# Performance work log

Hardware: AMD Instinct MI355X
Metric: run time of the kernel (lower is better)

## Reference

```python
import jax, jax.numpy as jnp
import numpy as np

N_NODES = 50000
N_EDGES = 800000
F_IN = 128
HEADS = 4
C_OUT = 32
NEG_SLOPE = 0.2
BN_EPS = 1e-5


def _add_self_loops(edge_index, edge_attr, n):
    # PyG fill_value='mean': self-loop attr = mean of incoming edge attrs per node (0 if none)
    src, dst = edge_index[0], edge_index[1]
    deg = jax.ops.segment_sum(jnp.ones_like(edge_attr[:, 0]), dst, num_segments=n)
    loop_attr = jax.ops.segment_sum(edge_attr, dst, num_segments=n) / jnp.maximum(deg, 1.0)[:, None]
    loop = jnp.arange(n)
    src2 = jnp.concatenate([src, loop])
    dst2 = jnp.concatenate([dst, loop])
    attr2 = jnp.concatenate([edge_attr, loop_attr], axis=0)
    return src2, dst2, attr2


def _segment_softmax(logits, seg, n):
    m = jax.ops.segment_max(logits, seg, num_segments=n)
    m = jnp.where(jnp.isfinite(m), m, 0.0)
    ex = jnp.exp(logits - m[seg])
    s = jax.ops.segment_sum(ex, seg, num_segments=n)
    return ex / s[seg]


def _gatv2(x, src, dst, eattr, Wl, bl, Wr, br, We, att, bias, n):
    # x: [n, F]; returns [n, HEADS*C_OUT]
    xl = (x @ Wl + bl).reshape(n, HEADS, C_OUT)
    xr = (x @ Wr + br).reshape(n, HEADS, C_OUT)
    ea = (eattr @ We).reshape(-1, HEADS, C_OUT)
    xlj = xl[src]                                   # [E, H, C] gather
    msg = jax.nn.leaky_relu(xlj + xr[dst] + ea, NEG_SLOPE)
    logits = jnp.einsum('ehc,hc->eh', msg, att)     # [E, H]
    alpha = _segment_softmax(logits, dst, n)
    out = jax.ops.segment_sum(xlj * alpha[..., None], dst, num_segments=n)
    return out.reshape(n, HEADS * C_OUT) + bias


def _batchnorm(x, gamma, beta):
    mu = x.mean(axis=0)
    var = x.var(axis=0)
    return gamma * (x - mu) * jax.lax.rsqrt(var + BN_EPS) + beta


def setup_inputs() -> dict:
    key = jax.random.key(0)
    ks = jax.random.split(key, 20)
    HC = HEADS * C_OUT
    s = 0.05
    inp = {
        'emb': jax.random.normal(ks[0], (N_NODES, F_IN), dtype=jnp.float32),
        'edge_index': jax.random.randint(ks[1], (2, N_EDGES), 0, N_NODES, dtype=jnp.int64),
        'edge_weight': jax.random.uniform(ks[2], (N_EDGES, 1), dtype=jnp.float32),
        'Wl1': jax.random.normal(ks[3], (F_IN, HC)) * s,
        'bl1': jnp.zeros((HC,), jnp.float32),
        'Wr1': jax.random.normal(ks[4], (F_IN, HC)) * s,
        'br1': jnp.zeros((HC,), jnp.float32),
        'We1': jax.random.normal(ks[5], (1, HC)) * s,
        'att1': jax.random.normal(ks[6], (HEADS, C_OUT)) * s,
        'bias1': jnp.zeros((HC,), jnp.float32),
        'gamma1': jnp.ones((HC,), jnp.float32),
        'beta1': jnp.zeros((HC,), jnp.float32),
        'Wl2': jax.random.normal(ks[7], (HC, HC)) * s,
        'bl2': jnp.zeros((HC,), jnp.float32),
        'Wr2': jax.random.normal(ks[8], (HC, HC)) * s,
        'br2': jnp.zeros((HC,), jnp.float32),
        'We2': jax.random.normal(ks[9], (1, HC)) * s,
        'att2': jax.random.normal(ks[10], (HEADS, C_OUT)) * s,
        'bias2': jnp.zeros((HC,), jnp.float32),
    }
    return inp


def reference(emb, edge_index, edge_weight, Wl1, bl1, Wr1, br1, We1, att1, bias1,
              gamma1, beta1, Wl2, bl2, Wr2, br2, We2, att2, bias2):
    n = emb.shape[0]
    src, dst, eattr = _add_self_loops(edge_index, edge_weight, n)
    h1 = _gatv2(emb, src, dst, eattr, Wl1, bl1, Wr1, br1, We1, att1, bias1, n)
    h1 = jax.nn.elu(_batchnorm(h1, gamma1, beta1))
    h2 = _gatv2(h1, src, dst, eattr, Wl2, bl2, Wr2, br2, We2, att2, bias2, n)
    # fusion: mean over [input_emb, h1, h2] along stacked axis
    return (emb + h1 + h2) / 3.0
```

## Files before the change

kernel.cpp:

```cpp
#include <hip/hip_runtime.h>
#include <hip/hip_bf16.h>
#include <math.h>

#define N_NODES 50000
#define N_EDGES 800000
#define HC 128
#define SLOT 64

#define BM 128
#define NBX ((N_NODES + BM - 1) / BM)

typedef short bh8 __attribute__((ext_vector_type(8)));
typedef float f4 __attribute__((ext_vector_type(4)));

__device__ __forceinline__ unsigned int pk2(float a, float b) {
  return (unsigned int)__bfloat16_as_ushort(__float2bfloat16(a)) |
         ((unsigned int)__bfloat16_as_ushort(__float2bfloat16(b)) << 16);
}

__global__ void k_wprep(const float* __restrict__ Wl1, const float* __restrict__ Wr1,
                        const float* __restrict__ Wl2, const float* __restrict__ Wr2,
                        unsigned short* __restrict__ WtAll) {
  int m = blockIdx.y;
  const float* src = (m == 0) ? Wl1 : (m == 1) ? Wr1 : (m == 2) ? Wl2 : Wr2;
  int idx = blockIdx.x * 256 + threadIdx.x;
  int k = idx >> 7, n = idx & 127;
  float v = src[k * HC + n];
  WtAll[((size_t)m * HC + n) * HC + k] = __bfloat16_as_ushort(__float2bfloat16(v));
}

__global__ void k_bucket(const int* __restrict__ ei, const float* __restrict__ ew,
                         int* __restrict__ cursor, int2* __restrict__ slots) {
  int e = blockIdx.x * blockDim.x + threadIdx.x;
  if (e >= N_EDGES) return;
  int s = ei[e];
  int d = ei[N_EDGES + e];
  float w = ew[e];
  int pos = atomicAdd(cursor + d, 1);
  if (pos < SLOT) {
    slots[(size_t)d * SLOT + pos] = make_int2(s, __float_as_int(w));
  }
}

template <int LAYER2>
__global__ __launch_bounds__(256) void k_gemm_mfma(
    const float* __restrict__ X, const unsigned short* __restrict__ Wt,
    const float* __restrict__ b0, const float* __restrict__ b1,
    unsigned short* __restrict__ Y0b, float* __restrict__ Y1,
    const float* __restrict__ scp, const float* __restrict__ shp) {
  __shared__ __align__(16) unsigned short Xls[128 * 128];
  __shared__ __align__(16) unsigned short Wls[128 * 128];
  int tid = threadIdx.x;
  int row0 = blockIdx.x * BM;
  {
    int r = tid >> 1;
    int ks = (tid & 1) * 64;
    int gr = row0 + r;
    const float* xp = X + (size_t)gr * HC + ks;
    int sw = r & 15;
#pragma unroll
    for (int i = 0; i < 4; ++i) {
      float f[16];
      if (gr < N_NODES) {
        *(float4*)&f[0] = *(const float4*)(xp + i * 16);
        *(float4*)&f[4] = *(const float4*)(xp + i * 16 + 4);
        *(float4*)&f[8] = *(const float4*)(xp + i * 16 + 8);
        *(float4*)&f[12] = *(const float4*)(xp + i * 16 + 12);
      } else {
#pragma unroll
        for (int j = 0; j < 16; ++j) f[j] = 0.f;
      }
      if (LAYER2) {
        float sc[16], sh[16];
#pragma unroll
        for (int q = 0; q < 4; ++q) {
          *(float4*)&sc[q * 4] = *(const float4*)(scp + ks + i * 16 + q * 4);
          *(float4*)&sh[q * 4] = *(const float4*)(shp + ks + i * 16 + q * 4);
        }
#pragma unroll
        for (int j = 0; j < 16; ++j) {
          float y = fmaf(f[j], sc[j], sh[j]);
          f[j] = (y > 0.f) ? y : (__expf(y) - 1.f);
        }
      }
      int kg = (ks >> 3) + i * 2;
      *(uint4*)&Xls[r * 128 + ((kg ^ sw) * 8)] =
          make_uint4(pk2(f[0], f[1]), pk2(f[2], f[3]), pk2(f[4], f[5]), pk2(f[6], f[7]));
      *(uint4*)&Xls[r * 128 + (((kg + 1) ^ sw) * 8)] =
          make_uint4(pk2(f[8], f[9]), pk2(f[10], f[11]), pk2(f[12], f[13]), pk2(f[14], f[15]));
    }
  }
  int lane = tid & 63;
  int wv = tid >> 6;
  int lrow = lane & 15;
  int lq = lane >> 4;
  int rbase = wv * 32;
#pragma unroll
  for (int half = 0; half < 2; ++half) {
    if (half) __syncthreads();
    {
      int n = tid >> 1;
      int ks = (tid & 1) * 64;
      const unsigned short* wp = Wt + half * (HC * HC) + n * HC + ks;
      int swn = n & 15;
#pragma unroll
      for (int g = 0; g < 8; ++g) {
        uint4 v = *(const uint4*)(wp + g * 8);
        int kg = (ks >> 3) + g;
        *(uint4*)&Wls[n * 128 + ((kg ^ swn) * 8)] = v;
      }
    }
    __syncthreads();
    f4 acc[2][8];
#pragma unroll
    for (int mt = 0; mt < 2; ++mt)
#pragma unroll
      for (int nt = 0; nt < 8; ++nt) acc[mt][nt] = (f4){0.f, 0.f, 0.f, 0.f};
#pragma unroll
    for (int kk = 0; kk < 4; ++kk) {
      int kg = kk * 4 + lq;
      bh8 a0 = *(const bh8*)&Xls[(rbase + lrow) * 128 + ((kg ^ lrow) * 8)];
      bh8 a1 = *(const bh8*)&Xls[(rbase + 16 + lrow) * 128 + ((kg ^ lrow) * 8)];
#pragma unroll
      for (int nt = 0; nt < 8; ++nt) {
        bh8 b = *(const bh8*)&Wls[(nt * 16 + lrow) * 128 + ((kg ^ lrow) * 8)];
        acc[0][nt] = __builtin_amdgcn_mfma_f32_16x16x32_bf16(a0, b, acc[0][nt], 0, 0, 0);
        acc[1][nt] = __builtin_amdgcn_mfma_f32_16x16x32_bf16(a1, b, acc[1][nt], 0, 0, 0);
      }
    }
    const float* bb = half ? b1 : b0;
    float bv[8];
#pragma unroll
    for (int nt = 0; nt < 8; ++nt) bv[nt] = bb[nt * 16 + lrow];
#pragma unroll
    for (int mt = 0; mt < 2; ++mt) {
#pragma unroll
      for (int rr = 0; rr < 4; ++rr) {
        int gr = row0 + rbase + mt * 16 + lq * 4 + rr;
        if (gr < N_NODES) {
          if (half == 0) {
#pragma unroll
            for (int nt = 0; nt < 8; ++nt)
              Y0b[(size_t)gr * HC + nt * 16 + lrow] =
                  __bfloat16_as_ushort(__float2bfloat16(acc[mt][nt][rr] + bv[nt]));
          } else {
#pragma unroll
            for (int nt = 0; nt < 8; ++nt)
              Y1[(size_t)gr * HC + nt * 16 + lrow] = acc[mt][nt][rr] + bv[nt];
          }
        }
      }
    }
  }
}

template <int FINAL>
__global__ __launch_bounds__(256) void k_gat(
    const unsigned short* __restrict__ xlb, const float* __restrict__ xr,
    const int* __restrict__ cursor, const int2* __restrict__ slots,
    const float* __restrict__ We, const float* __restrict__ att,
    const float* __restrict__ bias,
    float* __restrict__ out,
    const float* __restrict__ emb, const float* __restrict__ h1p,
    const float* __restrict__ scp, const float* __restrict__ shp) {
  int g = threadIdx.x >> 5;
  int lane = threadIdx.x & 31;
  int n = blockIdx.x * 8 + g;
  if (n >= N_NODES) return;
  int fi = n * 32 + lane;
  const uint2* xl4 = (const uint2*)xlb;
  float4 xr4 = ((const float4*)xr)[fi];
  float4 we4 = ((const float4*)We)[lane];
  float4 at4 = ((const float4*)att)[lane];
  int deg = min(cursor[n], SLOT);
  int jb = n * SLOT;
  int je = jb + deg;
  float l = 0.f, wsum = 0.f;
  float4 o = make_float4(0.f, 0.f, 0.f, 0.f);

  auto core = [&](float w, uint2 gc) {
    float4 xlj;
    xlj.x = __uint_as_float(gc.x << 16);
    xlj.y = __uint_as_float(gc.x & 0xffff0000u);
    xlj.z = __uint_as_float(gc.y << 16);
    xlj.w = __uint_as_float(gc.y & 0xffff0000u);
    float4 v;
    v.x = fmaf(w, we4.x, xlj.x + xr4.x);
    v.y = fmaf(w, we4.y, xlj.y + xr4.y);
    v.z = fmaf(w, we4.z, xlj.z + xr4.z);
    v.w = fmaf(w, we4.w, xlj.w + xr4.w);
    v.x = fmaxf(v.x, 0.2f * v.x);
    v.y = fmaxf(v.y, 0.2f * v.y);
    v.z = fmaxf(v.z, 0.2f * v.z);
    v.w = fmaxf(v.w, 0.2f * v.w);
    float p = v.x * at4.x + v.y * at4.y + v.z * at4.z + v.w * at4.w;
    p += __shfl_xor(p, 1);
    p += __shfl_xor(p, 2);
    p += __shfl_xor(p, 4);
    float e = __expf(p);
    l += e;
    o.x = fmaf(e, xlj.x, o.x);
    o.y = fmaf(e, xlj.y, o.y);
    o.z = fmaf(e, xlj.z, o.z);
    o.w = fmaf(e, xlj.w, o.w);
  };
  auto body = [&](int2 ec, uint2 gc) {
    float w = __int_as_float(ec.y);
    wsum += w;
    core(w, gc);
  };
  auto ld = [&](int j, int2& e, uint2& gq) {
    int idx = min(j, je - 1);
    e = slots[idx];
    gq = xl4[(size_t)e.x * 32 + lane];
  };

  if (deg > 0) {
    int2 e0, e1, e2, e3;
    uint2 g0, g1, g2, g3;
    ld(jb + 0, e0, g0);
    ld(jb + 1, e1, g1);
    ld(jb + 2, e2, g2);
    ld(jb + 3, e3, g3);
    for (int j = jb; j < je; j += 4) {
      int2 t0 = e0, t1 = e1, t2 = e2, t3 = e3;
      uint2 u0 = g0, u1 = g1, u2 = g2, u3 = g3;
      ld(j + 4, e0, g0);
      ld(j + 5, e1, g1);
      ld(j + 6, e2, g2);
      ld(j + 7, e3, g3);
      body(t0, u0);
      if (j + 1 < je) body(t1, u1);
      if (j + 2 < je) body(t2, u2);
      if (j + 3 < je) body(t3, u3);
    }
  }
  {
    float wself = (deg > 0) ? wsum / (float)deg : 0.f;
    uint2 gs = xl4[(size_t)n * 32 + lane];
    core(wself, gs);
  }

  float inv = 1.f / l;
  float4 b4 = ((const float4*)bias)[lane];
  float4 r;
  r.x = fmaf(o.x, inv, b4.x);
  r.y = fmaf(o.y, inv, b4.y);
  r.z = fmaf(o.z, inv, b4.z);
  r.w = fmaf(o.w, inv, b4.w);
  if (FINAL) {
    float4 e4 = ((const float4*)emb)[fi];
    float4 h4 = ((const float4*)h1p)[fi];
    float4 sc4 = ((const float4*)scp)[lane];
    float4 sh4 = ((const float4*)shp)[lane];
    float4 h;
    h.x = fmaf(h4.x, sc4.x, sh4.x);
    h.y = fmaf(h4.y, sc4.y, sh4.y);
    h.z = fmaf(h4.z, sc4.z, sh4.z);
    h.w = fmaf(h4.w, sc4.w, sh4.w);
    h.x = (h.x > 0.f) ? h.x : (__expf(h.x) - 1.f);
    h.y = (h.y > 0.f) ? h.y : (__expf(h.y) - 1.f);
    h.z = (h.z > 0.f) ? h.z : (__expf(h.z) - 1.f);
    h.w = (h.w > 0.f) ? h.w : (__expf(h.w) - 1.f);
    const float k3 = 1.f / 3.f;
    r.x = (e4.x + h.x + r.x) * k3;
    r.y = (e4.y + h.y + r.y) * k3;
    r.z = (e4.z + h.z + r.z) * k3;
    r.w = (e4.w + h.w + r.w) * k3;
  }
  ((float4*)out)[fi] = r;
}

#define BN_ROWS 200
__global__ __launch_bounds__(256) void k_bnstats(const float* __restrict__ h1,
                                                 float* __restrict__ chsum,
                                                 float* __restrict__ chsq) {
  int c = threadIdx.x & 127;
  int g = threadIdx.x >> 7;
  int r0 = blockIdx.x * BN_ROWS;
  float s = 0.f, q = 0.f;
  for (int r = r0 + g; r < r0 + BN_ROWS; r += 2) {
    float v = h1[(size_t)r * HC + c];
    s += v;
    q += v * v;
  }
  __shared__ float sh[256], shq[256];
  sh[threadIdx.x] = s;
  shq[threadIdx.x] = q;
  __syncthreads();
  if (g == 0) {
    atomicAdd(chsum + c, s + sh[threadIdx.x + 128]);
    atomicAdd(chsq + c, q + shq[threadIdx.x + 128]);
  }
}

__global__ void k_bnfin(float* __restrict__ chsum, float* __restrict__ chsq,
                        const float* __restrict__ gamma,
                        const float* __restrict__ beta) {
  int c = threadIdx.x;
  float mu = chsum[c] * (1.f / N_NODES);
  float var = chsq[c] * (1.f / N_NODES) - mu * mu;
  float sc = gamma[c] * rsqrtf(var + 1e-5f);
  chsum[c] = sc;
  chsq[c] = beta[c] - mu * sc;
}

extern "C" void kernel_launch(void* const* d_in, const int* in_sizes, int n_in,
                              void* d_out, int out_size, void* d_ws, size_t ws_size,
                              hipStream_t stream) {
  const float* emb = (const float*)d_in[0];
  const int* ei = (const int*)d_in[1];
  const float* ew = (const float*)d_in[2];
  const float* Wl1 = (const float*)d_in[3];
  const float* bl1 = (const float*)d_in[4];
  const float* Wr1 = (const float*)d_in[5];
  const float* br1 = (const float*)d_in[6];
  const float* We1 = (const float*)d_in[7];
  const float* att1 = (const float*)d_in[8];
  const float* bias1 = (const float*)d_in[9];
  const float* gamma1 = (const float*)d_in[10];
  const float* beta1 = (const float*)d_in[11];
  const float* Wl2 = (const float*)d_in[12];
  const float* bl2 = (const float*)d_in[13];
  const float* Wr2 = (const float*)d_in[14];
  const float* br2 = (const float*)d_in[15];
  const float* We2 = (const float*)d_in[16];
  const float* att2 = (const float*)d_in[17];
  const float* bias2 = (const float*)d_in[18];
  float* out = (float*)d_out;

  char* wsb = (char*)d_ws;
  size_t off = 0;
  auto alloc = [&](size_t bytes) -> void* {
    void* p = (void*)(wsb + off);
    off += (bytes + 255) & ~(size_t)255;
    return p;
  };
  int* cursor = (int*)alloc((size_t)N_NODES * 4);
  float* chsum = (float*)alloc(HC * 4);
  float* chsq = (float*)alloc(HC * 4);
  size_t zero_bytes = off;
  unsigned short* WtAll = (unsigned short*)alloc((size_t)4 * HC * HC * 2);
  int2* slots = (int2*)alloc((size_t)N_NODES * SLOT * 8);
  unsigned short* xlb = (unsigned short*)alloc((size_t)N_NODES * HC * 2);
  float* xr = (float*)alloc((size_t)N_NODES * HC * 4);
  float* h1 = (float*)alloc((size_t)N_NODES * HC * 4);

  hipMemsetAsync(d_ws, 0, zero_bytes, stream);

  k_wprep<<<dim3(64, 4), 256, 0, stream>>>(Wl1, Wr1, Wl2, Wr2, WtAll);
  k_bucket<<<(N_EDGES + 255) / 256, 256, 0, stream>>>(ei, ew, cursor, slots);

  k_gemm_mfma<0><<<NBX, 256, 0, stream>>>(emb, WtAll, bl1, br1, xlb, xr,
                                          nullptr, nullptr);
  k_gat<0><<<N_NODES / 8, 256, 0, stream>>>(xlb, xr, cursor, slots, We1, att1,
                                            bias1, h1, nullptr, nullptr, nullptr,
                                            nullptr);
  k_bnstats<<<N_NODES / BN_ROWS, 256, 0, stream>>>(h1, chsum, chsq);
  k_bnfin<<<1, HC, 0, stream>>>(chsum, chsq, gamma1, beta1);
  k_gemm_mfma<1><<<NBX, 256, 0, stream>>>(h1, WtAll + 2 * HC * HC, bl2, br2,
                                          xlb, xr, chsum, chsq);
  k_gat<1><<<N_NODES / 8, 256, 0, stream>>>(xlb, xr, cursor, slots, We2, att2,
                                            bias2, out, emb, h1, chsum, chsq);
}
```

Baseline: 327.1 us.

## Merge prep kernels, fold BN finalize into consumers, warp-load GAT edge lists

Combines the weight-transpose and edge-bucketing kernels into one launch, and drops the separate BN finalize kernel by recomputing scale and shift inside the layer-2 GEMM (via shared memory) and the final GAT kernel. The GAT kernel now has lanes load up to 32 edge slots cooperatively, reduce the edge-weight sum with shuffles, and broadcast source indices via __shfl, so per-edge slot loads no longer sit on the critical path. Edges beyond 32 fall back to a serial loop. The cost is redundant BN finalize math in every block and a changed loop structure with masked tail iterations.

```diff
diff --git a/kernel.cpp b/kernel.cpp
--- a/kernel.cpp
+++ b/kernel.cpp
@@ -9,6 +9,8 @@
 
 #define BM 128
 #define NBX ((N_NODES + BM - 1) / BM)
+#define NB_WPREP 256
+#define NB_BUCKET ((N_EDGES + 255) / 256)
 
 typedef short bh8 __attribute__((ext_vector_type(8)));
 typedef float f4 __attribute__((ext_vector_type(4)));
@@ -18,20 +20,22 @@
          ((unsigned int)__bfloat16_as_ushort(__float2bfloat16(b)) << 16);
 }
 
-__global__ void k_wprep(const float* __restrict__ Wl1, const float* __restrict__ Wr1,
-                        const float* __restrict__ Wl2, const float* __restrict__ Wr2,
-                        unsigned short* __restrict__ WtAll) {
-  int m = blockIdx.y;
-  const float* src = (m == 0) ? Wl1 : (m == 1) ? Wr1 : (m == 2) ? Wl2 : Wr2;
-  int idx = blockIdx.x * 256 + threadIdx.x;
-  int k = idx >> 7, n = idx & 127;
-  float v = src[k * HC + n];
-  WtAll[((size_t)m * HC + n) * HC + k] = __bfloat16_as_ushort(__float2bfloat16(v));
-}
-
-__global__ void k_bucket(const int* __restrict__ ei, const float* __restrict__ ew,
-                         int* __restrict__ cursor, int2* __restrict__ slots) {
-  int e = blockIdx.x * blockDim.x + threadIdx.x;
+__global__ void k_prep(const float* __restrict__ Wl1, const float* __restrict__ Wr1,
+                       const float* __restrict__ Wl2, const float* __restrict__ Wr2,
+                       unsigned short* __restrict__ WtAll,
+                       const int* __restrict__ ei, const float* __restrict__ ew,
+                       int* __restrict__ cursor, int2* __restrict__ slots) {
+  int bid = blockIdx.x;
+  if (bid < NB_WPREP) {
+    int m = bid >> 6;
+    const float* src = (m == 0) ? Wl1 : (m == 1) ? Wr1 : (m == 2) ? Wl2 : Wr2;
+    int idx = (bid & 63) * 256 + threadIdx.x;
+    int k = idx >> 7, n = idx & 127;
+    WtAll[((size_t)m * HC + n) * HC + k] =
+        __bfloat16_as_ushort(__float2bfloat16(src[k * HC + n]));
+    return;
+  }
+  int e = (bid - NB_WPREP) * 256 + threadIdx.x;
   if (e >= N_EDGES) return;
   int s = ei[e];
   int d = ei[N_EDGES + e];
@@ -47,10 +51,22 @@
     const float* __restrict__ X, const unsigned short* __restrict__ Wt,
     const float* __restrict__ b0, const float* __restrict__ b1,
     unsigned short* __restrict__ Y0b, float* __restrict__ Y1,
-    const float* __restrict__ scp, const float* __restrict__ shp) {
+    const float* __restrict__ chsum, const float* __restrict__ chsq,
+    const float* __restrict__ gamma, const float* __restrict__ beta) {
   __shared__ __align__(16) unsigned short Xls[128 * 128];
   __shared__ __align__(16) unsigned short Wls[128 * 128];
+  __shared__ float ssc[HC], ssh[HC];
   int tid = threadIdx.x;
+  if (LAYER2) {
+    if (tid < HC) {
+      float mu = chsum[tid] * (1.f / N_NODES);
+      float var = chsq[tid] * (1.f / N_NODES) - mu * mu;
+      float sc = gamma[tid] * rsqrtf(var + 1e-5f);
+      ssc[tid] = sc;
+      ssh[tid] = beta[tid] - mu * sc;
+    }
+    __syncthreads();
+  }
   int row0 = blockIdx.x * BM;
   {
     int r = tid >> 1;
@@ -71,15 +87,9 @@
         for (int j = 0; j < 16; ++j) f[j] = 0.f;
       }
       if (LAYER2) {
-        float sc[16], sh[16];
-#pragma unroll
-        for (int q = 0; q < 4; ++q) {
-          *(float4*)&sc[q * 4] = *(const float4*)(scp + ks + i * 16 + q * 4);
-          *(float4*)&sh[q * 4] = *(const float4*)(shp + ks + i * 16 + q * 4);
-        }
 #pragma unroll
         for (int j = 0; j < 16; ++j) {
-          float y = fmaf(f[j], sc[j], sh[j]);
+          float y = fmaf(f[j], ssc[ks + i * 16 + j], ssh[ks + i * 16 + j]);
           f[j] = (y > 0.f) ? y : (__expf(y) - 1.f);
         }
       }
@@ -159,26 +169,37 @@
     const unsigned short* __restrict__ xlb, const float* __restrict__ xr,
     const int* __restrict__ cursor, const int2* __restrict__ slots,
     const float* __restrict__ We, const float* __restrict__ att,
-    const float* __restrict__ bias,
-    float* __restrict__ out,
+    const float* __restrict__ bias, float* __restrict__ out,
     const float* __restrict__ emb, const float* __restrict__ h1p,
-    const float* __restrict__ scp, const float* __restrict__ shp) {
+    const float* __restrict__ chsum, const float* __restrict__ chsq,
+    const float* __restrict__ gamma, const float* __restrict__ beta) {
   int g = threadIdx.x >> 5;
   int lane = threadIdx.x & 31;
   int n = blockIdx.x * 8 + g;
-  if (n >= N_NODES) return;
   int fi = n * 32 + lane;
   const uint2* xl4 = (const uint2*)xlb;
   float4 xr4 = ((const float4*)xr)[fi];
   float4 we4 = ((const float4*)We)[lane];
   float4 at4 = ((const float4*)att)[lane];
   int deg = min(cursor[n], SLOT);
-  int jb = n * SLOT;
-  int je = jb + deg;
-  float l = 0.f, wsum = 0.f;
+  int base = n * SLOT;
+  int deg32 = min(deg, 32);
+
+  int evs = 0;
+  float evw = 0.f;
+  if (lane < deg32) {
+    int2 ev = slots[base + lane];
+    evs = ev.x;
+    evw = __int_as_float(ev.y);
+  }
+  float wsum = evw;
+#pragma unroll
+  for (int m = 16; m >= 1; m >>= 1) wsum += __shfl_xor(wsum, m);
+
+  float l = 0.f;
   float4 o = make_float4(0.f, 0.f, 0.f, 0.f);
 
-  auto core = [&](float w, uint2 gc) {
+  auto edge_body = [&](float w, uint2 gc, bool valid) {
     float4 xlj;
     xlj.x = __uint_as_float(gc.x << 16);
     xlj.y = __uint_as_float(gc.x & 0xffff0000u);
@@ -197,48 +218,52 @@
     p += __shfl_xor(p, 1);
     p += __shfl_xor(p, 2);
     p += __shfl_xor(p, 4);
-    float e = __expf(p);
+    float e = valid ? __expf(p) : 0.f;
     l += e;
     o.x = fmaf(e, xlj.x, o.x);
     o.y = fmaf(e, xlj.y, o.y);
     o.z = fmaf(e, xlj.z, o.z);
     o.w = fmaf(e, xlj.w, o.w);
   };
-  auto body = [&](int2 ec, uint2 gc) {
-    float w = __int_as_float(ec.y);
-    wsum += w;
-    core(w, gc);
+  auto fetch = [&](int j, uint2& qq, float& ww) {
+    int jc = min(j, deg32 - 1);
+    int s = __shfl(evs, jc, 32);
+    ww = __shfl(evw, jc, 32);
+    qq = xl4[s * 32 + lane];
   };
-  auto ld = [&](int j, int2& e, uint2& gq) {
-    int idx = min(j, je - 1);
-    e = slots[idx];
-    gq = xl4[(size_t)e.x * 32 + lane];
-  };
-
-  if (deg > 0) {
-    int2 e0, e1, e2, e3;
-    uint2 g0, g1, g2, g3;
-    ld(jb + 0, e0, g0);
-    ld(jb + 1, e1, g1);
-    ld(jb + 2, e2, g2);
-    ld(jb + 3, e3, g3);
-    for (int j = jb; j < je; j += 4) {
-      int2 t0 = e0, t1 = e1, t2 = e2, t3 = e3;
-      uint2 u0 = g0, u1 = g1, u2 = g2, u3 = g3;
-      ld(j + 4, e0, g0);
-      ld(j + 5, e1, g1);
-      ld(j + 6, e2, g2);
-      ld(j + 7, e3, g3);
-      body(t0, u0);
-      if (j + 1 < je) body(t1, u1);
-      if (j + 2 < je) body(t2, u2);
-      if (j + 3 < je) body(t3, u3);
+
+  if (deg32 > 0) {
+    uint2 q0, q1, q2, q3;
+    float w0, w1, w2, w3;
+    fetch(0, q0, w0);
+    fetch(1, q1, w1);
+    fetch(2, q2, w2);
+    fetch(3, q3, w3);
+    for (int b = 0; b < deg32; b += 4) {
+      uint2 c0 = q0, c1 = q1, c2 = q2, c3 = q3;
+      float x0 = w0, x1 = w1, x2 = w2, x3 = w3;
+      fetch(b + 4, q0, w0);
+      fetch(b + 5, q1, w1);
+      fetch(b + 6, q2, w2);
+      fetch(b + 7, q3, w3);
+      edge_body(x0, c0, true);
+      edge_body(x1, c1, b + 1 < deg32);
+      edge_body(x2, c2, b + 2 < deg32);
+      edge_body(x3, c3, b + 3 < deg32);
+    }
+  }
+  if (deg > 32) {
+    for (int j = base + 32; j < base + deg; ++j) {
+      int2 e = slots[j];
+      float w = __int_as_float(e.y);
+      wsum += w;
+      uint2 gc = xl4[e.x * 32 + lane];
+      edge_body(w, gc, true);
     }
   }
   {
     float wself = (deg > 0) ? wsum / (float)deg : 0.f;
-    uint2 gs = xl4[(size_t)n * 32 + lane];
-    core(wself, gs);
+    edge_body(wself, xl4[n * 32 + lane], true);
   }
 
   float inv = 1.f / l;
@@ -251,8 +276,22 @@
   if (FINAL) {
     float4 e4 = ((const float4*)emb)[fi];
     float4 h4 = ((const float4*)h1p)[fi];
-    float4 sc4 = ((const float4*)scp)[lane];
-    float4 sh4 = ((const float4*)shp)[lane];
+    float4 cs = ((const float4*)chsum)[lane];
+    float4 cq = ((const float4*)chsq)[lane];
+    float4 gm = ((const float4*)gamma)[lane];
+    float4 bt = ((const float4*)beta)[lane];
+    const float invN = 1.f / N_NODES;
+    float4 sc4, sh4;
+    {
+      float mu = cs.x * invN, var = cq.x * invN - mu * mu;
+      sc4.x = gm.x * rsqrtf(var + 1e-5f); sh4.x = bt.x - mu * sc4.x;
+      mu = cs.y * invN; var = cq.y * invN - mu * mu;
+      sc4.y = gm.y * rsqrtf(var + 1e-5f); sh4.y = bt.y - mu * sc4.y;
+      mu = cs.z * invN; var = cq.z * invN - mu * mu;
+      sc4.z = gm.z * rsqrtf(var + 1e-5f); sh4.z = bt.z - mu * sc4.z;
+      mu = cs.w * invN; var = cq.w * invN - mu * mu;
+      sc4.w = gm.w * rsqrtf(var + 1e-5f); sh4.w = bt.w - mu * sc4.w;
+    }
     float4 h;
     h.x = fmaf(h4.x, sc4.x, sh4.x);
     h.y = fmaf(h4.y, sc4.y, sh4.y);
@@ -292,17 +331,6 @@
     atomicAdd(chsum + c, s + sh[threadIdx.x + 128]);
     atomicAdd(chsq + c, q + shq[threadIdx.x + 128]);
   }
-}
-
-__global__ void k_bnfin(float* __restrict__ chsum, float* __restrict__ chsq,
-                        const float* __restrict__ gamma,
-                        const float* __restrict__ beta) {
-  int c = threadIdx.x;
-  float mu = chsum[c] * (1.f / N_NODES);
-  float var = chsq[c] * (1.f / N_NODES) - mu * mu;
-  float sc = gamma[c] * rsqrtf(var + 1e-5f);
-  chsum[c] = sc;
-  chsq[c] = beta[c] - mu * sc;
 }
 
 extern "C" void kernel_launch(void* const* d_in, const int* in_sizes, int n_in,
@@ -348,18 +376,17 @@
 
   hipMemsetAsync(d_ws, 0, zero_bytes, stream);
 
-  k_wprep<<<dim3(64, 4), 256, 0, stream>>>(Wl1, Wr1, Wl2, Wr2, WtAll);
-  k_bucket<<<(N_EDGES + 255) / 256, 256, 0, stream>>>(ei, ew, cursor, slots);
-
+  k_prep<<<NB_WPREP + NB_BUCKET, 256, 0, stream>>>(Wl1, Wr1, Wl2, Wr2, WtAll,
+                                                   ei, ew, cursor, slots);
   k_gemm_mfma<0><<<NBX, 256, 0, stream>>>(emb, WtAll, bl1, br1, xlb, xr,
-                                          nullptr, nullptr);
+                                          nullptr, nullptr, nullptr, nullptr);
   k_gat<0><<<N_NODES / 8, 256, 0, stream>>>(xlb, xr, cursor, slots, We1, att1,
                                             bias1, h1, nullptr, nullptr, nullptr,
-                                            nullptr);
+                                            nullptr, nullptr, nullptr);
   k_bnstats<<<N_NODES / BN_ROWS, 256, 0, stream>>>(h1, chsum, chsq);
-  k_bnfin<<<1, HC, 0, stream>>>(chsum, chsq, gamma1, beta1);
   k_gemm_mfma<1><<<NBX, 256, 0, stream>>>(h1, WtAll + 2 * HC * HC, bl2, br2,
-                                          xlb, xr, chsum, chsq);
+                                          xlb, xr, chsum, chsq, gamma1, beta1);
   k_gat<1><<<N_NODES / 8, 256, 0, stream>>>(xlb, xr, cursor, slots, We2, att2,
-                                            bias2, out, emb, h1, chsum, chsq);
-}
+                                            bias2, out, emb, h1, chsum, chsq,
+                                            gamma1, beta1);
+}
```

Measured after the change: 308.0 us. 5.8% less time.
